# Kernel tuning notes

Measured on AMD Instinct MI355X. Metric: run time of the kernel, lower is better.

## Reference

```python
import jax, jax.numpy as jnp
import numpy as np

DMODEL = 512
NUM_HEADS = 8
HEAD_DIM = DMODEL // NUM_HEADS


def setup_inputs() -> dict:
    key = jax.random.key(0)
    k1, k2, k3, k4, k5 = jax.random.split(key, 5)
    x = jax.random.normal(k1, (4, 2048, DMODEL), dtype=jnp.float32)
    s = 1.0 / np.sqrt(DMODEL)
    W_qkv = jax.random.uniform(k2, (DMODEL, 3 * DMODEL), jnp.float32, -s, s)
    b_qkv = jax.random.uniform(k3, (3 * DMODEL,), jnp.float32, -s, s)
    W_out = jax.random.uniform(k4, (DMODEL, DMODEL), jnp.float32, -s, s)
    b_out = jax.random.uniform(k5, (DMODEL,), jnp.float32, -s, s)
    return {"x": x, "W_qkv": W_qkv, "b_qkv": b_qkv, "W_out": W_out, "b_out": b_out}


def reference(x, W_qkv, b_qkv, W_out, b_out):
    B, T, D = x.shape
    H, Hd = NUM_HEADS, HEAD_DIM
    qkv = x @ W_qkv + b_qkv                      # [B, T, 3D]
    qkv = qkv.reshape(B, T, 3, H, Hd).transpose(2, 0, 3, 1, 4)  # [3, B, H, T, Hd]
    q, k, v = qkv[0], qkv[1], qkv[2]
    scores = jnp.einsum('bhqd,bhkd->bhqk', q, k) / np.sqrt(Hd)  # [B, H, T, T]
    causal = jnp.tril(jnp.ones((T, T), dtype=bool))
    scores = jnp.where(causal, scores, -jnp.inf)
    weights = jax.nn.softmax(scores, axis=-1)
    out = jnp.einsum('bhqk,bhkd->bhqd', weights, v)  # [B, H, T, Hd]
    out = out.transpose(0, 2, 1, 3).reshape(B, T, D)
    return out @ W_out + b_out
```

## Files before the change

### kernel.cpp

```cpp
#include <hip/hip_runtime.h>
#include <cstdint>
#include <cstddef>

#define D_MODEL 512
#define SEQ_T 2048
#define NHEADS 8
#define HDIM 64

typedef __attribute__((ext_vector_type(8))) short bf16x8;
typedef __attribute__((ext_vector_type(4))) float f32x4;

__device__ __forceinline__ unsigned short f2bf(float f) {
  unsigned int u = __float_as_uint(f);
  u += 0x7FFFu + ((u >> 16) & 1u);
  return (unsigned short)(u >> 16);
}

__device__ __forceinline__ unsigned int pack_bf16(float lo, float hi) {
  unsigned int a = __float_as_uint(lo) + 0x8000u;
  unsigned int b = __float_as_uint(hi) + 0x8000u;
  return __builtin_amdgcn_perm(b, a, 0x07060302u);
}

#define QSCALE 0.18033688011112043f
#define SSHIFT 16.0f

__device__ __forceinline__ void async_lds16(const unsigned short* g,
                                            unsigned short* l) {
  __builtin_amdgcn_global_load_lds(
      (const __attribute__((address_space(1))) void*)g,
      (__attribute__((address_space(3))) void*)l, 16, 0, 0);
}

__global__ __launch_bounds__(256) void prep_kernel(
    const float* __restrict__ x, const float* __restrict__ W_qkv,
    const float* __restrict__ W_out, unsigned short* __restrict__ xb,
    unsigned short* __restrict__ Wqkt, unsigned short* __restrict__ Wot) {
  __shared__ float tile[64][65];
  const int bid = blockIdx.x;
  if (bid < 2048) {
    int i = (bid * 256 + threadIdx.x) * 8;
    float4 a = *(const float4*)(x + i);
    float4 b = *(const float4*)(x + i + 4);
    ushort4 lo = {f2bf(a.x), f2bf(a.y), f2bf(a.z), f2bf(a.w)};
    ushort4 hi = {f2bf(b.x), f2bf(b.y), f2bf(b.z), f2bf(b.w)};
    *(ushort4*)(xb + i) = lo;
    *(ushort4*)(xb + i + 4) = hi;
    return;
  }
  const float* src;
  unsigned short* dst;
  int R = 512, C, c0, r0;
  if (bid < 2048 + 192) {
    int t = bid - 2048;
    C = 1536; c0 = (t % 24) * 64; r0 = (t / 24) * 64;
    src = W_qkv; dst = Wqkt;
  } else {
    int t = bid - 2240;
    C = 512; c0 = (t & 7) * 64; r0 = (t >> 3) * 64;
    src = W_out; dst = Wot;
  }
  for (int i = threadIdx.x; i < 64 * 64; i += 256) {
    int r = i >> 6, c = i & 63;
    tile[r][c] = src[(size_t)(r0 + r) * C + c0 + c];
  }
  __syncthreads();
  for (int i = threadIdx.x; i < 64 * 64; i += 256) {
    int c = i >> 6, r = i & 63;
    dst[(size_t)(c0 + c) * R + r0 + r] = f2bf(tile[r][c]);
  }
}

__global__ __launch_bounds__(256) void gemm_qkv_mfma(
    const unsigned short* __restrict__ xb, const unsigned short* __restrict__ Wt,
    const float* __restrict__ bias, unsigned short* __restrict__ Qtb,
    unsigned short* __restrict__ Kb, unsigned short* __restrict__ Vtb) {
  __shared__ unsigned short As[128 * 64];
  __shared__ unsigned short Bs[128 * 64];
  const int tid = threadIdx.x;
  const int w = tid >> 6, lane = tid & 63;
  const int quad = lane >> 4, l15 = lane & 15;
  const int wm = w >> 1, wn = w & 1;
  const int m0 = blockIdx.x * 128, n0 = blockIdx.y * 128;

  const int srow = tid >> 3;
  const int schunk = (tid & 7) ^ (srow & 7);
  const unsigned short* ga = xb + (size_t)(m0 + srow) * 512 + schunk * 8;
  const unsigned short* gb = Wt + (size_t)(n0 + srow) * 512 + schunk * 8;
  unsigned short* lA = As + tid * 8;
  unsigned short* lB = Bs + tid * 8;

  f32x4 acc[4][4] = {};
  for (int k0 = 0; k0 < 512; k0 += 64) {
#pragma unroll
    for (int rr = 0; rr < 4; ++rr) {
      async_lds16(ga + (size_t)rr * 32 * 512 + k0, lA + rr * 2048);
      async_lds16(gb + (size_t)rr * 32 * 512 + k0, lB + rr * 2048);
    }
    __syncthreads();
    bf16x8 af[4][2], bfr[4][2];
#pragma unroll
    for (int mb = 0; mb < 4; ++mb) {
      int row = wm * 64 + mb * 16 + l15;
#pragma unroll
      for (int kk = 0; kk < 2; ++kk) {
        int slot = (kk * 4 + quad) ^ (row & 7);
        af[mb][kk] = *(const bf16x8*)&As[row * 64 + slot * 8];
      }
    }
#pragma unroll
    for (int nb = 0; nb < 4; ++nb) {
      int row = wn * 64 + nb * 16 + l15;
#pragma unroll
      for (int kk = 0; kk < 2; ++kk) {
        int slot = (kk * 4 + quad) ^ (row & 7);
        bfr[nb][kk] = *(const bf16x8*)&Bs[row * 64 + slot * 8];
      }
    }
#pragma unroll
    for (int mb = 0; mb < 4; ++mb)
#pragma unroll
      for (int nb = 0; nb < 4; ++nb) {
        acc[mb][nb] = __builtin_amdgcn_mfma_f32_16x16x32_bf16(
            af[mb][0], bfr[nb][0], acc[mb][nb], 0, 0, 0);
        acc[mb][nb] = __builtin_amdgcn_mfma_f32_16x16x32_bf16(
            af[mb][1], bfr[nb][1], acc[mb][nb], 0, 0, 0);
      }
    __syncthreads();
  }

  const int cbase = n0 + wn * 64;
  const int three = cbase >> 9;
  const int h = (cbase >> 6) & 7;
  const int bh = ((m0 >> 11) << 3) + h;
  const int t0 = (m0 & 2047) + wm * 64;
  float bv[4];
#pragma unroll
  for (int nb = 0; nb < 4; ++nb) bv[nb] = bias[cbase + nb * 16 + l15];

  if (three == 0) {
#pragma unroll
    for (int mb = 0; mb < 4; ++mb)
#pragma unroll
      for (int nb = 0; nb < 4; ++nb) {
        int trow = t0 + mb * 16 + quad * 4;
        ushort4 v = {f2bf((acc[mb][nb][0] + bv[nb]) * QSCALE),
                     f2bf((acc[mb][nb][1] + bv[nb]) * QSCALE),
                     f2bf((acc[mb][nb][2] + bv[nb]) * QSCALE),
                     f2bf((acc[mb][nb][3] + bv[nb]) * QSCALE)};
        *(ushort4*)(Qtb + ((size_t)bh * HDIM + nb * 16 + l15) * SEQ_T + trow) = v;
      }
  } else if (three == 2) {
#pragma unroll
    for (int mb = 0; mb < 4; ++mb)
#pragma unroll
      for (int nb = 0; nb < 4; ++nb) {
        int trow = t0 + mb * 16 + quad * 4;
        ushort4 v = {f2bf(acc[mb][nb][0] + bv[nb]), f2bf(acc[mb][nb][1] + bv[nb]),
                     f2bf(acc[mb][nb][2] + bv[nb]), f2bf(acc[mb][nb][3] + bv[nb])};
        *(ushort4*)(Vtb + ((size_t)bh * HDIM + nb * 16 + l15) * SEQ_T + trow) = v;
      }
  } else {
#pragma unroll
    for (int mb = 0; mb < 4; ++mb)
#pragma unroll
      for (int nb = 0; nb < 4; ++nb)
#pragma unroll
        for (int r = 0; r < 4; ++r) {
          int trow = t0 + mb * 16 + quad * 4 + r;
          Kb[((size_t)bh * SEQ_T + trow) * HDIM + nb * 16 + l15] =
              f2bf(acc[mb][nb][r] + bv[nb]);
        }
  }
}

__global__ __launch_bounds__(256, 4) void attn_mfma5(
    const unsigned short* __restrict__ Qtb, const unsigned short* __restrict__ Kb,
    const unsigned short* __restrict__ Vtb, unsigned short* __restrict__ AOb) {
  __shared__ __align__(16) unsigned short Ks[2][64 * 64];
  __shared__ __align__(16) unsigned short Vs[2][64 * 64];
  __shared__ __align__(16) unsigned short Pt[4][16 * 64];
  const int tid = threadIdx.x;
  const int w = tid >> 6, lane = tid & 63;
  const int quad = lane >> 4, l15 = lane & 15;

  const int bid = blockIdx.x;
  const int xcd = bid & 7;
  const int j = bid >> 3;
  const int c = j & 31, g = j >> 5;
  const int k = c >> 2;
  const int bh = xcd + 8 * (c & 3);
  const int qt = (g == 0) ? (31 - k) : (g == 1) ? (16 + k)
               : (g == 2) ? (15 - k) : k;

  const unsigned short* kbase = Kb + (size_t)bh * SEQ_T * HDIM;
  const unsigned short* vbase = Vtb + (size_t)bh * HDIM * SEQ_T;
  const int sr = tid >> 3;
  const int lc = tid & 7;
  const int scol = lc * 8;
  const int swc = (lc ^ (sr & 7)) * 8;

  bf16x8 qf0, qf1;
  {
    unsigned short qraw[16];
    const unsigned short* qp =
        Qtb + ((size_t)bh * HDIM + quad * 8) * SEQ_T + qt * 64 + w * 16 + l15;
#pragma unroll
    for (int jj = 0; jj < 8; ++jj) {
      qraw[jj] = qp[(size_t)jj * SEQ_T];
      qraw[8 + jj] = qp[(size_t)(32 + jj) * SEQ_T];
    }
    qf0 = *(const bf16x8*)qraw;
    qf1 = *(const bf16x8*)(qraw + 8);
  }
  const short oneb = (short)0x3F80;
  const bf16x8 ones = {oneb, oneb, oneb, oneb, oneb, oneb, oneb, oneb};

  f32x4 O[4] = {{0.f, 0.f, 0.f, 0.f}, {0.f, 0.f, 0.f, 0.f},
                {0.f, 0.f, 0.f, 0.f}, {0.f, 0.f, 0.f, 0.f}};
  f32x4 l_acc = {0.f, 0.f, 0.f, 0.f};
  const int q_rel = w * 16 + l15;
  const int r7 = l15 & 7;

  uint4 rk0, rk1, rv0, rv1;
  {
    const unsigned short* kp = kbase + (size_t)sr * 64 + scol;
    rk0 = *(const uint4*)kp;
    rk1 = *(const uint4*)(kp + 32 * 64);
    const unsigned short* vp = vbase + (size_t)sr * SEQ_T + scol;
    rv0 = *(const uint4*)vp;
    rv1 = *(const uint4*)(vp + 32 * SEQ_T);
  }
  *(uint4*)&Ks[0][sr * 64 + swc] = rk0;
  *(uint4*)&Ks[0][(sr + 32) * 64 + swc] = rk1;
  *(uint4*)&Vs[0][sr * 64 + swc] = rv0;
  *(uint4*)&Vs[0][(sr + 32) * 64 + swc] = rv1;
  __syncthreads();

  for (int i = 0; i < qt; ++i) {
    const int cur = i & 1;
    {
      const int nkt = i + 1;
      const unsigned short* kp = kbase + (size_t)(nkt * 64 + sr) * 64 + scol;
      rk0 = *(const uint4*)kp;
      rk1 = *(const uint4*)(kp + 32 * 64);
      const unsigned short* vp = vbase + (size_t)sr * SEQ_T + nkt * 64 + scol;
      rv0 = *(const uint4*)vp;
      rv1 = *(const uint4*)(vp + 32 * SEQ_T);
    }

    f32x4 S[4];
#pragma unroll
    for (int nb = 0; nb < 4; ++nb) {
      const int row = nb * 16 + l15;
      const unsigned short* k0p = &Ks[cur][row * 64 + ((quad ^ r7) * 8)];
      const unsigned short* k1p = &Ks[cur][row * 64 + (((quad + 4) ^ r7) * 8)];
      f32x4 z = {0.f, 0.f, 0.f, 0.f};
      z = __builtin_amdgcn_mfma_f32_16x16x32_bf16(*(const bf16x8*)k0p, qf0, z,
                                                  0, 0, 0);
      S[nb] = __builtin_amdgcn_mfma_f32_16x16x32_bf16(*(const bf16x8*)k1p, qf1,
                                                      z, 0, 0, 0);
    }

#pragma unroll
    for (int nb = 0; nb < 4; ++nb) {
      float p0 = __builtin_amdgcn_exp2f(S[nb][0] - SSHIFT);
      float p1 = __builtin_amdgcn_exp2f(S[nb][1] - SSHIFT);
      float p2 = __builtin_amdgcn_exp2f(S[nb][2] - SSHIFT);
      float p3 = __builtin_amdgcn_exp2f(S[nb][3] - SSHIFT);
      int cc = 2 * nb + (quad >> 1);
      uint2 pk = {pack_bf16(p0, p1), pack_bf16(p2, p3)};
      *(uint2*)&Pt[w][l15 * 64 + ((cc ^ r7) * 8) + (quad & 1) * 4] = pk;
    }

    bf16x8 pb0 = *(const bf16x8*)&Pt[w][l15 * 64 + ((quad ^ r7) * 8)];
    bf16x8 pb1 = *(const bf16x8*)&Pt[w][l15 * 64 + (((quad + 4) ^ r7) * 8)];
    l_acc = __builtin_amdgcn_mfma_f32_16x16x32_bf16(ones, pb0, l_acc, 0, 0, 0);
    l_acc = __builtin_amdgcn_mfma_f32_16x16x32_bf16(ones, pb1, l_acc, 0, 0, 0);
#pragma unroll
    for (int nbd = 0; nbd < 4; ++nbd) {
      const int row = nbd * 16 + l15;
      const unsigned short* v0p = &Vs[cur][row * 64 + ((quad ^ r7) * 8)];
      const unsigned short* v1p = &Vs[cur][row * 64 + (((quad + 4) ^ r7) * 8)];
      O[nbd] = __builtin_amdgcn_mfma_f32_16x16x32_bf16(*(const bf16x8*)v0p, pb0,
                                                       O[nbd], 0, 0, 0);
      O[nbd] = __builtin_amdgcn_mfma_f32_16x16x32_bf16(*(const bf16x8*)v1p, pb1,
                                                       O[nbd], 0, 0, 0);
    }

    const int nxt = cur ^ 1;
    *(uint4*)&Ks[nxt][sr * 64 + swc] = rk0;
    *(uint4*)&Ks[nxt][(sr + 32) * 64 + swc] = rk1;
    *(uint4*)&Vs[nxt][sr * 64 + swc] = rv0;
    *(uint4*)&Vs[nxt][(sr + 32) * 64 + swc] = rv1;
    __syncthreads();
  }

  {
    const int cur = qt & 1;
    const int nb_lim = w + 1;
    f32x4 S[4];
#pragma unroll
    for (int nb = 0; nb < 4; ++nb) {
      if (nb < nb_lim) {
        const int row = nb * 16 + l15;
        const unsigned short* k0p = &Ks[cur][row * 64 + ((quad ^ r7) * 8)];
        const unsigned short* k1p =
            &Ks[cur][row * 64 + (((quad + 4) ^ r7) * 8)];
        f32x4 z = {0.f, 0.f, 0.f, 0.f};
        z = __builtin_amdgcn_mfma_f32_16x16x32_bf16(*(const bf16x8*)k0p, qf0,
                                                    z, 0, 0, 0);
        S[nb] = __builtin_amdgcn_mfma_f32_16x16x32_bf16(*(const bf16x8*)k1p,
                                                        qf1, z, 0, 0, 0);
      }
    }
#pragma unroll
    for (int nb = 0; nb < 4; ++nb) {
      int cc = 2 * nb + (quad >> 1);
      if (nb < nb_lim) {
        float pp[4];
#pragma unroll
        for (int r = 0; r < 4; ++r) {
          float p = __builtin_amdgcn_exp2f(S[nb][r] - SSHIFT);
          int key_rel = nb * 16 + quad * 4 + r;
          pp[r] = (key_rel > q_rel) ? 0.f : p;
        }
        uint2 pk = {pack_bf16(pp[0], pp[1]), pack_bf16(pp[2], pp[3])};
        *(uint2*)&Pt[w][l15 * 64 + ((cc ^ r7) * 8) + (quad & 1) * 4] = pk;
      } else {
        uint2 z2 = {0u, 0u};
        *(uint2*)&Pt[w][l15 * 64 + ((cc ^ r7) * 8) + (quad & 1) * 4] = z2;
      }
    }
    const int kpv = (w >= 2) ? 2 : 1;
    bf16x8 pb0 = *(const bf16x8*)&Pt[w][l15 * 64 + ((quad ^ r7) * 8)];
    bf16x8 pb1 = *(const bf16x8*)&Pt[w][l15 * 64 + (((quad + 4) ^ r7) * 8)];
    l_acc = __builtin_amdgcn_mfma_f32_16x16x32_bf16(ones, pb0, l_acc, 0, 0, 0);
    if (kpv == 2)
      l_acc =
          __builtin_amdgcn_mfma_f32_16x16x32_bf16(ones, pb1, l_acc, 0, 0, 0);
#pragma unroll
    for (int nbd = 0; nbd < 4; ++nbd) {
      const int row = nbd * 16 + l15;
      const unsigned short* v0p = &Vs[cur][row * 64 + ((quad ^ r7) * 8)];
      O[nbd] = __builtin_amdgcn_mfma_f32_16x16x32_bf16(*(const bf16x8*)v0p, pb0,
                                                       O[nbd], 0, 0, 0);
      if (kpv == 2) {
        const unsigned short* v1p =
            &Vs[cur][row * 64 + (((quad + 4) ^ r7) * 8)];
        O[nbd] = __builtin_amdgcn_mfma_f32_16x16x32_bf16(*(const bf16x8*)v1p,
                                                         pb1, O[nbd], 0, 0, 0);
      }
    }
  }

  float inv = 1.0f / l_acc[0];
  const int bb = bh >> 3, h = bh & 7;
  int qrow = qt * 64 + q_rel;
  unsigned short* dst = AOb + ((size_t)bb * SEQ_T + qrow) * D_MODEL + (h << 6);
#pragma unroll
  for (int nbd = 0; nbd < 4; ++nbd) {
    ushort4 o4 = {f2bf(O[nbd][0] * inv), f2bf(O[nbd][1] * inv),
                  f2bf(O[nbd][2] * inv), f2bf(O[nbd][3] * inv)};
    *(ushort4*)(dst + nbd * 16 + quad * 4) = o4;
  }
}

__global__ __launch_bounds__(256) void gemm_out_mfma(
    const unsigned short* __restrict__ AOb, const unsigned short* __restrict__ Wot,
    const float* __restrict__ bias, float* __restrict__ out) {
  __shared__ unsigned short As[64 * 64];
  __shared__ unsigned short Bs[128 * 64];
  const int tid = threadIdx.x;
  const int w = tid >> 6, lane = tid & 63;
  const int quad = lane >> 4, l15 = lane & 15;
  const int m0 = blockIdx.x * 64, n0 = blockIdx.y * 128;

  const int srow = tid >> 3;
  const int schunk = (tid & 7) ^ (srow & 7);
  const unsigned short* ga = AOb + (size_t)(m0 + srow) * 512 + schunk * 8;
  const unsigned short* gb = Wot + (size_t)(n0 + srow) * 512 + schunk * 8;
  unsigned short* lA = As + tid * 8;
  unsigned short* lB = Bs + tid * 8;

  f32x4 acc[4][2] = {};
  for (int k0 = 0; k0 < 512; k0 += 64) {
#pragma unroll
    for (int rr = 0; rr < 2; ++rr)
      async_lds16(ga + (size_t)rr * 32 * 512 + k0, lA + rr * 2048);
#pragma unroll
    for (int rr = 0; rr < 4; ++rr)
      async_lds16(gb + (size_t)rr * 32 * 512 + k0, lB + rr * 2048);
    __syncthreads();
    bf16x8 af[4][2], bfr[2][2];
#pragma unroll
    for (int mb = 0; mb < 4; ++mb) {
      int row = mb * 16 + l15;
#pragma unroll
      for (int kk = 0; kk < 2; ++kk) {
        int slot = (kk * 4 + quad) ^ (row & 7);
        af[mb][kk] = *(const bf16x8*)&As[row * 64 + slot * 8];
      }
    }
#pragma unroll
    for (int nb = 0; nb < 2; ++nb) {
      int row = w * 32 + nb * 16 + l15;
#pragma unroll
      for (int kk = 0; kk < 2; ++kk) {
        int slot = (kk * 4 + quad) ^ (row & 7);
        bfr[nb][kk] = *(const bf16x8*)&Bs[row * 64 + slot * 8];
      }
    }
#pragma unroll
    for (int mb = 0; mb < 4; ++mb)
#pragma unroll
      for (int nb = 0; nb < 2; ++nb) {
        acc[mb][nb] = __builtin_amdgcn_mfma_f32_16x16x32_bf16(
            af[mb][0], bfr[nb][0], acc[mb][nb], 0, 0, 0);
        acc[mb][nb] = __builtin_amdgcn_mfma_f32_16x16x32_bf16(
            af[mb][1], bfr[nb][1], acc[mb][nb], 0, 0, 0);
      }
    __syncthreads();
  }

  const int cbase = n0 + w * 32;
  float bv[2];
#pragma unroll
  for (int nb = 0; nb < 2; ++nb) bv[nb] = bias[cbase + nb * 16 + l15];
#pragma unroll
  for (int mb = 0; mb < 4; ++mb)
#pragma unroll
    for (int nb = 0; nb < 2; ++nb)
#pragma unroll
      for (int r = 0; r < 4; ++r)
        out[(size_t)(m0 + mb * 16 + quad * 4 + r) * 512 + cbase + nb * 16 +
            l15] = acc[mb][nb][r] + bv[nb];
}

extern "C" void kernel_launch(void* const* d_in, const int* in_sizes, int n_in,
                              void* d_out, int out_size, void* d_ws,
                              size_t ws_size, hipStream_t stream) {
  const float* x     = (const float*)d_in[0];
  const float* W_qkv = (const float*)d_in[1];
  const float* b_qkv = (const float*)d_in[2];
  const float* W_out = (const float*)d_in[3];
  const float* b_out = (const float*)d_in[4];
  float* out = (float*)d_out;

  const size_t NX = (size_t)4 * SEQ_T * D_MODEL;
  unsigned short* xb   = (unsigned short*)d_ws;
  unsigned short* Wqkt = xb + NX;
  unsigned short* Wot  = Wqkt + (size_t)1536 * 512;
  unsigned short* Qtb  = Wot + (size_t)512 * 512;
  unsigned short* Kb   = Qtb + NX;
  unsigned short* Vtb  = Kb + NX;
  unsigned short* AOb  = Vtb + NX;

  prep_kernel<<<2304, 256, 0, stream>>>(x, W_qkv, W_out, xb, Wqkt, Wot);
  gemm_qkv_mfma<<<dim3(64, 12), 256, 0, stream>>>(xb, Wqkt, b_qkv, Qtb, Kb,
                                                  Vtb);
  attn_mfma5<<<dim3(1024), 256, 0, stream>>>(Qtb, Kb, Vtb, AOb);
  gemm_out_mfma<<<dim3(128, 4), 256, 0, stream>>>(AOb, Wot, b_out, out);
}
```

Baseline: 132.8 us.

## Process two query tiles per attention block to reuse K/V tiles

Each attention block now handles 128 query rows (two 64-row sub-tiles) against each staged K/V tile, so every K/V tile loaded into LDS feeds twice the MFMA work and the grid is halved. The causal diagonal is handled with per-subtile modes: masked, skipped or full. The aim is to cut global K/V traffic and LDS staging per query. In exchange the kernel uses twice the accumulator and P-tile LDS, its occupancy hint drops to 3, and with half as many blocks the load balancing across CUs gets coarser.

Result: slower. 143.4 us (+8.0%).

```diff
diff --git a/kernel.cpp b/kernel.cpp
--- a/kernel.cpp
+++ b/kernel.cpp
@@ -174,24 +174,23 @@
   }
 }
 
-__global__ __launch_bounds__(256, 4) void attn_mfma5(
+__global__ __launch_bounds__(256, 3) void attn_mfma6(
     const unsigned short* __restrict__ Qtb, const unsigned short* __restrict__ Kb,
     const unsigned short* __restrict__ Vtb, unsigned short* __restrict__ AOb) {
   __shared__ __align__(16) unsigned short Ks[2][64 * 64];
   __shared__ __align__(16) unsigned short Vs[2][64 * 64];
-  __shared__ __align__(16) unsigned short Pt[4][16 * 64];
+  __shared__ __align__(16) unsigned short Pt[4 * 2048];
   const int tid = threadIdx.x;
   const int w = tid >> 6, lane = tid & 63;
   const int quad = lane >> 4, l15 = lane & 15;
 
   const int bid = blockIdx.x;
   const int xcd = bid & 7;
-  const int j = bid >> 3;
-  const int c = j & 31, g = j >> 5;
-  const int k = c >> 2;
+  const int rest = bid >> 3;
+  const int c = rest & 31, g = rest >> 5;
   const int bh = xcd + 8 * (c & 3);
-  const int qt = (g == 0) ? (31 - k) : (g == 1) ? (16 + k)
-               : (g == 2) ? (15 - k) : k;
+  const int kq = c >> 2;
+  const int qt = g ? kq : (15 - kq);
 
   const unsigned short* kbase = Kb + (size_t)bh * SEQ_T * HDIM;
   const unsigned short* vbase = Vtb + (size_t)bh * HDIM * SEQ_T;
@@ -200,27 +199,33 @@
   const int scol = lc * 8;
   const int swc = (lc ^ (sr & 7)) * 8;
 
-  bf16x8 qf0, qf1;
-  {
+  bf16x8 qf[2][2];
+#pragma unroll
+  for (int h = 0; h < 2; ++h) {
     unsigned short qraw[16];
-    const unsigned short* qp =
-        Qtb + ((size_t)bh * HDIM + quad * 8) * SEQ_T + qt * 64 + w * 16 + l15;
+    const unsigned short* qp = Qtb + ((size_t)bh * HDIM + quad * 8) * SEQ_T +
+                               qt * 128 + h * 64 + w * 16 + l15;
 #pragma unroll
     for (int jj = 0; jj < 8; ++jj) {
       qraw[jj] = qp[(size_t)jj * SEQ_T];
       qraw[8 + jj] = qp[(size_t)(32 + jj) * SEQ_T];
     }
-    qf0 = *(const bf16x8*)qraw;
-    qf1 = *(const bf16x8*)(qraw + 8);
+    qf[h][0] = *(const bf16x8*)qraw;
+    qf[h][1] = *(const bf16x8*)(qraw + 8);
   }
   const short oneb = (short)0x3F80;
   const bf16x8 ones = {oneb, oneb, oneb, oneb, oneb, oneb, oneb, oneb};
 
-  f32x4 O[4] = {{0.f, 0.f, 0.f, 0.f}, {0.f, 0.f, 0.f, 0.f},
-                {0.f, 0.f, 0.f, 0.f}, {0.f, 0.f, 0.f, 0.f}};
-  f32x4 l_acc = {0.f, 0.f, 0.f, 0.f};
+  f32x4 O[2][4];
+  f32x4 l_acc[2];
+#pragma unroll
+  for (int h = 0; h < 2; ++h) {
+    l_acc[h] = (f32x4){0.f, 0.f, 0.f, 0.f};
+#pragma unroll
+    for (int nbd = 0; nbd < 4; ++nbd) O[h][nbd] = (f32x4){0.f, 0.f, 0.f, 0.f};
+  }
   const int q_rel = w * 16 + l15;
-  const int r7 = l15 & 7;
+  const int r7m = l15 & 7;
 
   uint4 rk0, rk1, rv0, rv1;
   {
@@ -237,132 +242,142 @@
   *(uint4*)&Vs[0][(sr + 32) * 64 + swc] = rv1;
   __syncthreads();
 
-  for (int i = 0; i < qt; ++i) {
-    const int cur = i & 1;
-    {
-      const int nkt = i + 1;
-      const unsigned short* kp = kbase + (size_t)(nkt * 64 + sr) * 64 + scol;
-      rk0 = *(const uint4*)kp;
-      rk1 = *(const uint4*)(kp + 32 * 64);
-      const unsigned short* vp = vbase + (size_t)sr * SEQ_T + nkt * 64 + scol;
-      rv0 = *(const uint4*)vp;
-      rv1 = *(const uint4*)(vp + 32 * SEQ_T);
-    }
-
-    f32x4 S[4];
-#pragma unroll
-    for (int nb = 0; nb < 4; ++nb) {
-      const int row = nb * 16 + l15;
-      const unsigned short* k0p = &Ks[cur][row * 64 + ((quad ^ r7) * 8)];
-      const unsigned short* k1p = &Ks[cur][row * 64 + (((quad + 4) ^ r7) * 8)];
-      f32x4 z = {0.f, 0.f, 0.f, 0.f};
-      z = __builtin_amdgcn_mfma_f32_16x16x32_bf16(*(const bf16x8*)k0p, qf0, z,
-                                                  0, 0, 0);
-      S[nb] = __builtin_amdgcn_mfma_f32_16x16x32_bf16(*(const bf16x8*)k1p, qf1,
-                                                      z, 0, 0, 0);
-    }
-
-#pragma unroll
-    for (int nb = 0; nb < 4; ++nb) {
-      float p0 = __builtin_amdgcn_exp2f(S[nb][0] - SSHIFT);
-      float p1 = __builtin_amdgcn_exp2f(S[nb][1] - SSHIFT);
-      float p2 = __builtin_amdgcn_exp2f(S[nb][2] - SSHIFT);
-      float p3 = __builtin_amdgcn_exp2f(S[nb][3] - SSHIFT);
-      int cc = 2 * nb + (quad >> 1);
-      uint2 pk = {pack_bf16(p0, p1), pack_bf16(p2, p3)};
-      *(uint2*)&Pt[w][l15 * 64 + ((cc ^ r7) * 8) + (quad & 1) * 4] = pk;
-    }
-
-    bf16x8 pb0 = *(const bf16x8*)&Pt[w][l15 * 64 + ((quad ^ r7) * 8)];
-    bf16x8 pb1 = *(const bf16x8*)&Pt[w][l15 * 64 + (((quad + 4) ^ r7) * 8)];
-    l_acc = __builtin_amdgcn_mfma_f32_16x16x32_bf16(ones, pb0, l_acc, 0, 0, 0);
-    l_acc = __builtin_amdgcn_mfma_f32_16x16x32_bf16(ones, pb1, l_acc, 0, 0, 0);
-#pragma unroll
-    for (int nbd = 0; nbd < 4; ++nbd) {
-      const int row = nbd * 16 + l15;
-      const unsigned short* v0p = &Vs[cur][row * 64 + ((quad ^ r7) * 8)];
-      const unsigned short* v1p = &Vs[cur][row * 64 + (((quad + 4) ^ r7) * 8)];
-      O[nbd] = __builtin_amdgcn_mfma_f32_16x16x32_bf16(*(const bf16x8*)v0p, pb0,
-                                                       O[nbd], 0, 0, 0);
-      O[nbd] = __builtin_amdgcn_mfma_f32_16x16x32_bf16(*(const bf16x8*)v1p, pb1,
-                                                       O[nbd], 0, 0, 0);
-    }
-
-    const int nxt = cur ^ 1;
+  auto prefetch = [&](int nkt) {
+    const unsigned short* kp = kbase + (size_t)(nkt * 64 + sr) * 64 + scol;
+    rk0 = *(const uint4*)kp;
+    rk1 = *(const uint4*)(kp + 32 * 64);
+    const unsigned short* vp = vbase + (size_t)sr * SEQ_T + nkt * 64 + scol;
+    rv0 = *(const uint4*)vp;
+    rv1 = *(const uint4*)(vp + 32 * SEQ_T);
+  };
+  auto commit = [&](int nxt) {
     *(uint4*)&Ks[nxt][sr * 64 + swc] = rk0;
     *(uint4*)&Ks[nxt][(sr + 32) * 64 + swc] = rk1;
     *(uint4*)&Vs[nxt][sr * 64 + swc] = rv0;
     *(uint4*)&Vs[nxt][(sr + 32) * 64 + swc] = rv1;
-    __syncthreads();
-  }
-
-  {
-    const int cur = qt & 1;
-    const int nb_lim = w + 1;
-    f32x4 S[4];
+  };
+
+  auto tile_body = [&](int cur, int mode0, int mode1) {
+    const int lim0 = (mode0 == 2) ? 0 : ((mode0 == 1) ? (w + 1) : 4);
+    const int lim1 = (mode1 == 2) ? 0 : ((mode1 == 1) ? (w + 1) : 4);
+    f32x4 S0[4], S1[4];
 #pragma unroll
     for (int nb = 0; nb < 4; ++nb) {
-      if (nb < nb_lim) {
-        const int row = nb * 16 + l15;
-        const unsigned short* k0p = &Ks[cur][row * 64 + ((quad ^ r7) * 8)];
-        const unsigned short* k1p =
-            &Ks[cur][row * 64 + (((quad + 4) ^ r7) * 8)];
+      const int row = nb * 16 + l15;
+      bf16x8 k0 = *(const bf16x8*)&Ks[cur][row * 64 + ((quad ^ r7m) * 8)];
+      bf16x8 k1 = *(const bf16x8*)&Ks[cur][row * 64 + (((quad + 4) ^ r7m) * 8)];
+      if (nb < lim0) {
         f32x4 z = {0.f, 0.f, 0.f, 0.f};
-        z = __builtin_amdgcn_mfma_f32_16x16x32_bf16(*(const bf16x8*)k0p, qf0,
-                                                    z, 0, 0, 0);
-        S[nb] = __builtin_amdgcn_mfma_f32_16x16x32_bf16(*(const bf16x8*)k1p,
-                                                        qf1, z, 0, 0, 0);
-      }
-    }
-#pragma unroll
-    for (int nb = 0; nb < 4; ++nb) {
-      int cc = 2 * nb + (quad >> 1);
-      if (nb < nb_lim) {
-        float pp[4];
-#pragma unroll
-        for (int r = 0; r < 4; ++r) {
-          float p = __builtin_amdgcn_exp2f(S[nb][r] - SSHIFT);
-          int key_rel = nb * 16 + quad * 4 + r;
-          pp[r] = (key_rel > q_rel) ? 0.f : p;
+        z = __builtin_amdgcn_mfma_f32_16x16x32_bf16(k0, qf[0][0], z, 0, 0, 0);
+        S0[nb] = __builtin_amdgcn_mfma_f32_16x16x32_bf16(k1, qf[0][1], z, 0, 0, 0);
+      }
+      if (nb < lim1) {
+        f32x4 z = {0.f, 0.f, 0.f, 0.f};
+        z = __builtin_amdgcn_mfma_f32_16x16x32_bf16(k0, qf[1][0], z, 0, 0, 0);
+        S1[nb] = __builtin_amdgcn_mfma_f32_16x16x32_bf16(k1, qf[1][1], z, 0, 0, 0);
+      }
+    }
+#pragma unroll
+    for (int h = 0; h < 2; ++h) {
+      f32x4* S = h ? S1 : S0;
+      const int lim = h ? lim1 : lim0;
+      const int mode = h ? mode1 : mode0;
+#pragma unroll
+      for (int nb = 0; nb < 4; ++nb) {
+        int cc = 2 * nb + (quad >> 1);
+        unsigned short* base = &Pt[w * 2048 + h * 1024 + l15 * 64 +
+                                   ((cc ^ r7m) * 8) + (quad & 1) * 4];
+        if (nb < lim) {
+          float pp[4];
+#pragma unroll
+          for (int r = 0; r < 4; ++r) {
+            float p = __builtin_amdgcn_exp2f(S[nb][r] - SSHIFT);
+            if (mode == 1) {
+              int key_rel = nb * 16 + quad * 4 + r;
+              if (key_rel > q_rel) p = 0.f;
+            }
+            pp[r] = p;
+          }
+          uint2 pk = {pack_bf16(pp[0], pp[1]), pack_bf16(pp[2], pp[3])};
+          *(uint2*)base = pk;
+        } else if (mode == 1) {
+          uint2 z2 = {0u, 0u};
+          *(uint2*)base = z2;
         }
-        uint2 pk = {pack_bf16(pp[0], pp[1]), pack_bf16(pp[2], pp[3])};
-        *(uint2*)&Pt[w][l15 * 64 + ((cc ^ r7) * 8) + (quad & 1) * 4] = pk;
-      } else {
-        uint2 z2 = {0u, 0u};
-        *(uint2*)&Pt[w][l15 * 64 + ((cc ^ r7) * 8) + (quad & 1) * 4] = z2;
-      }
-    }
-    const int kpv = (w >= 2) ? 2 : 1;
-    bf16x8 pb0 = *(const bf16x8*)&Pt[w][l15 * 64 + ((quad ^ r7) * 8)];
-    bf16x8 pb1 = *(const bf16x8*)&Pt[w][l15 * 64 + (((quad + 4) ^ r7) * 8)];
-    l_acc = __builtin_amdgcn_mfma_f32_16x16x32_bf16(ones, pb0, l_acc, 0, 0, 0);
-    if (kpv == 2)
-      l_acc =
-          __builtin_amdgcn_mfma_f32_16x16x32_bf16(ones, pb1, l_acc, 0, 0, 0);
+      }
+    }
+    bf16x8 pb[2][2];
+    const int kpv0 = (mode0 == 1 && w < 2) ? 1 : 2;
+    const int kpv1 = (mode1 == 1 && w < 2) ? 1 : 2;
+    if (mode0 != 2) {
+      pb[0][0] = *(const bf16x8*)&Pt[w * 2048 + l15 * 64 + ((quad ^ r7m) * 8)];
+      pb[0][1] =
+          *(const bf16x8*)&Pt[w * 2048 + l15 * 64 + (((quad + 4) ^ r7m) * 8)];
+      l_acc[0] =
+          __builtin_amdgcn_mfma_f32_16x16x32_bf16(ones, pb[0][0], l_acc[0], 0, 0, 0);
+      if (kpv0 == 2)
+        l_acc[0] = __builtin_amdgcn_mfma_f32_16x16x32_bf16(ones, pb[0][1],
+                                                           l_acc[0], 0, 0, 0);
+    }
+    if (mode1 != 2) {
+      pb[1][0] =
+          *(const bf16x8*)&Pt[w * 2048 + 1024 + l15 * 64 + ((quad ^ r7m) * 8)];
+      pb[1][1] = *(const bf16x8*)&Pt[w * 2048 + 1024 + l15 * 64 +
+                                     (((quad + 4) ^ r7m) * 8)];
+      l_acc[1] =
+          __builtin_amdgcn_mfma_f32_16x16x32_bf16(ones, pb[1][0], l_acc[1], 0, 0, 0);
+      if (kpv1 == 2)
+        l_acc[1] = __builtin_amdgcn_mfma_f32_16x16x32_bf16(ones, pb[1][1],
+                                                           l_acc[1], 0, 0, 0);
+    }
 #pragma unroll
     for (int nbd = 0; nbd < 4; ++nbd) {
       const int row = nbd * 16 + l15;
-      const unsigned short* v0p = &Vs[cur][row * 64 + ((quad ^ r7) * 8)];
-      O[nbd] = __builtin_amdgcn_mfma_f32_16x16x32_bf16(*(const bf16x8*)v0p, pb0,
-                                                       O[nbd], 0, 0, 0);
-      if (kpv == 2) {
-        const unsigned short* v1p =
-            &Vs[cur][row * 64 + (((quad + 4) ^ r7) * 8)];
-        O[nbd] = __builtin_amdgcn_mfma_f32_16x16x32_bf16(*(const bf16x8*)v1p,
-                                                         pb1, O[nbd], 0, 0, 0);
-      }
-    }
-  }
-
-  float inv = 1.0f / l_acc[0];
-  const int bb = bh >> 3, h = bh & 7;
-  int qrow = qt * 64 + q_rel;
-  unsigned short* dst = AOb + ((size_t)bb * SEQ_T + qrow) * D_MODEL + (h << 6);
-#pragma unroll
-  for (int nbd = 0; nbd < 4; ++nbd) {
-    ushort4 o4 = {f2bf(O[nbd][0] * inv), f2bf(O[nbd][1] * inv),
-                  f2bf(O[nbd][2] * inv), f2bf(O[nbd][3] * inv)};
-    *(ushort4*)(dst + nbd * 16 + quad * 4) = o4;
+      bf16x8 v0 = *(const bf16x8*)&Vs[cur][row * 64 + ((quad ^ r7m) * 8)];
+      bf16x8 v1 = *(const bf16x8*)&Vs[cur][row * 64 + (((quad + 4) ^ r7m) * 8)];
+      if (mode0 != 2) {
+        O[0][nbd] = __builtin_amdgcn_mfma_f32_16x16x32_bf16(v0, pb[0][0],
+                                                            O[0][nbd], 0, 0, 0);
+        if (kpv0 == 2)
+          O[0][nbd] = __builtin_amdgcn_mfma_f32_16x16x32_bf16(
+              v1, pb[0][1], O[0][nbd], 0, 0, 0);
+      }
+      if (mode1 != 2) {
+        O[1][nbd] = __builtin_amdgcn_mfma_f32_16x16x32_bf16(v0, pb[1][0],
+                                                            O[1][nbd], 0, 0, 0);
+        if (kpv1 == 2)
+          O[1][nbd] = __builtin_amdgcn_mfma_f32_16x16x32_bf16(
+              v1, pb[1][1], O[1][nbd], 0, 0, 0);
+      }
+    }
+  };
+
+  for (int i = 0; i < 2 * qt; ++i) {
+    const int cur = i & 1;
+    prefetch(i + 1);
+    tile_body(cur, 0, 0);
+    commit(cur ^ 1);
+    __syncthreads();
+  }
+  prefetch(2 * qt + 1);
+  tile_body(0, 1, 0);
+  commit(1);
+  __syncthreads();
+  tile_body(1, 2, 1);
+
+  const int bb = bh >> 3, h8 = bh & 7;
+#pragma unroll
+  for (int h = 0; h < 2; ++h) {
+    float inv = 1.0f / l_acc[h][0];
+    int qrow = qt * 128 + h * 64 + q_rel;
+    unsigned short* dst =
+        AOb + ((size_t)bb * SEQ_T + qrow) * D_MODEL + (h8 << 6);
+#pragma unroll
+    for (int nbd = 0; nbd < 4; ++nbd) {
+      ushort4 o4 = {f2bf(O[h][nbd][0] * inv), f2bf(O[h][nbd][1] * inv),
+                    f2bf(O[h][nbd][2] * inv), f2bf(O[h][nbd][3] * inv)};
+      *(ushort4*)(dst + nbd * 16 + quad * 4) = o4;
+    }
   }
 }
 
@@ -459,6 +474,6 @@
   prep_kernel<<<2304, 256, 0, stream>>>(x, W_qkv, W_out, xb, Wqkt, Wot);
   gemm_qkv_mfma<<<dim3(64, 12), 256, 0, stream>>>(xb, Wqkt, b_qkv, Qtb, Kb,
                                                   Vtb);
-  attn_mfma5<<<dim3(1024), 256, 0, stream>>>(Qtb, Kb, Vtb, AOb);
+  attn_mfma6<<<dim3(512), 256, 0, stream>>>(Qtb, Kb, Vtb, AOb);
   gemm_out_mfma<<<dim3(128, 4), 256, 0, stream>>>(AOb, Wot, b_out, out);
 }
```

## Split attention key tiles across waves and keep P in registers

Applied to the files above, without the earlier changes.

The attention kernel now gives each wave one 16-key slice of every 64-key tile for all 64 queries, where before each wave owned 16 queries over all keys. The softmax probabilities feed a 16x16x16 MFMA straight from registers, which removes the per-wave LDS round-trip for P and the ones-matrix MFMA used for row sums. The diagonal tile is folded into the main loop with masking. The cost is a cross-wave reduction of O and l through shared memory at the end, more registers (launch bounds lowered from 4 to 3 blocks), and more MFMA instructions for the PV product.

Result: slower. 142.3 us (+7.1%).

```diff
diff --git a/kernel.cpp b/kernel.cpp
--- a/kernel.cpp
+++ b/kernel.cpp
@@ -8,6 +8,7 @@
 #define HDIM 64
 
 typedef __attribute__((ext_vector_type(8))) short bf16x8;
+typedef __attribute__((ext_vector_type(4))) short bf16x4;
 typedef __attribute__((ext_vector_type(4))) float f32x4;
 
 __device__ __forceinline__ unsigned short f2bf(float f) {
@@ -174,12 +175,11 @@
   }
 }
 
-__global__ __launch_bounds__(256, 4) void attn_mfma5(
+__global__ __launch_bounds__(256, 3) void attn_mfma7(
     const unsigned short* __restrict__ Qtb, const unsigned short* __restrict__ Kb,
     const unsigned short* __restrict__ Vtb, unsigned short* __restrict__ AOb) {
-  __shared__ __align__(16) unsigned short Ks[2][64 * 64];
-  __shared__ __align__(16) unsigned short Vs[2][64 * 64];
-  __shared__ __align__(16) unsigned short Pt[4][16 * 64];
+  __shared__ __align__(16) unsigned short KVs[4][64 * 64];
+  __shared__ float ls[4 * 64];
   const int tid = threadIdx.x;
   const int w = tid >> 6, lane = tid & 63;
   const int quad = lane >> 4, l15 = lane & 15;
@@ -200,27 +200,33 @@
   const int scol = lc * 8;
   const int swc = (lc ^ (sr & 7)) * 8;
 
-  bf16x8 qf0, qf1;
-  {
-    unsigned short qraw[16];
-    const unsigned short* qp =
-        Qtb + ((size_t)bh * HDIM + quad * 8) * SEQ_T + qt * 64 + w * 16 + l15;
-#pragma unroll
-    for (int jj = 0; jj < 8; ++jj) {
-      qraw[jj] = qp[(size_t)jj * SEQ_T];
-      qraw[8 + jj] = qp[(size_t)(32 + jj) * SEQ_T];
-    }
-    qf0 = *(const bf16x8*)qraw;
-    qf1 = *(const bf16x8*)(qraw + 8);
-  }
-  const short oneb = (short)0x3F80;
-  const bf16x8 ones = {oneb, oneb, oneb, oneb, oneb, oneb, oneb, oneb};
-
-  f32x4 O[4] = {{0.f, 0.f, 0.f, 0.f}, {0.f, 0.f, 0.f, 0.f},
-                {0.f, 0.f, 0.f, 0.f}, {0.f, 0.f, 0.f, 0.f}};
-  f32x4 l_acc = {0.f, 0.f, 0.f, 0.f};
-  const int q_rel = w * 16 + l15;
-  const int r7 = l15 & 7;
+  bf16x8 qf[4][2];
+#pragma unroll
+  for (int qb = 0; qb < 4; ++qb) {
+#pragma unroll
+    for (int h = 0; h < 2; ++h) {
+      unsigned short qraw[8];
+      const unsigned short* qp = Qtb +
+          ((size_t)bh * HDIM + h * 32 + quad * 8) * SEQ_T + qt * 64 + qb * 16 +
+          l15;
+#pragma unroll
+      for (int jj = 0; jj < 8; ++jj) qraw[jj] = qp[(size_t)jj * SEQ_T];
+      qf[qb][h] = *(const bf16x8*)qraw;
+    }
+  }
+
+  f32x4 O[4][4];
+#pragma unroll
+  for (int dvb = 0; dvb < 4; ++dvb)
+#pragma unroll
+    for (int qb = 0; qb < 4; ++qb) O[dvb][qb] = (f32x4){0.f, 0.f, 0.f, 0.f};
+  float l4[4] = {0.f, 0.f, 0.f, 0.f};
+
+  const int myrowK = w * 16 + l15;
+  const int kc0 = (quad ^ (myrowK & 7)) * 8;
+  const int kc1 = ((quad + 4) ^ (myrowK & 7)) * 8;
+  const int vchunk = 2 * w + (quad >> 1);
+  const int vsub = (quad & 1) * 4;
 
   uint4 rk0, rk1, rv0, rv1;
   {
@@ -231,15 +237,17 @@
     rv0 = *(const uint4*)vp;
     rv1 = *(const uint4*)(vp + 32 * SEQ_T);
   }
-  *(uint4*)&Ks[0][sr * 64 + swc] = rk0;
-  *(uint4*)&Ks[0][(sr + 32) * 64 + swc] = rk1;
-  *(uint4*)&Vs[0][sr * 64 + swc] = rv0;
-  *(uint4*)&Vs[0][(sr + 32) * 64 + swc] = rv1;
+  *(uint4*)&KVs[0][sr * 64 + swc] = rk0;
+  *(uint4*)&KVs[0][(sr + 32) * 64 + swc] = rk1;
+  *(uint4*)&KVs[2][sr * 64 + swc] = rv0;
+  *(uint4*)&KVs[2][(sr + 32) * 64 + swc] = rv1;
   __syncthreads();
 
-  for (int i = 0; i < qt; ++i) {
+  for (int i = 0; i <= qt; ++i) {
     const int cur = i & 1;
-    {
+    const bool diag = (i == qt);
+
+    if (i < qt) {
       const int nkt = i + 1;
       const unsigned short* kp = kbase + (size_t)(nkt * 64 + sr) * 64 + scol;
       rk0 = *(const uint4*)kp;
@@ -249,120 +257,99 @@
       rv1 = *(const uint4*)(vp + 32 * SEQ_T);
     }
 
-    f32x4 S[4];
-#pragma unroll
-    for (int nb = 0; nb < 4; ++nb) {
-      const int row = nb * 16 + l15;
-      const unsigned short* k0p = &Ks[cur][row * 64 + ((quad ^ r7) * 8)];
-      const unsigned short* k1p = &Ks[cur][row * 64 + (((quad + 4) ^ r7) * 8)];
-      f32x4 z = {0.f, 0.f, 0.f, 0.f};
-      z = __builtin_amdgcn_mfma_f32_16x16x32_bf16(*(const bf16x8*)k0p, qf0, z,
-                                                  0, 0, 0);
-      S[nb] = __builtin_amdgcn_mfma_f32_16x16x32_bf16(*(const bf16x8*)k1p, qf1,
-                                                      z, 0, 0, 0);
-    }
-
-#pragma unroll
-    for (int nb = 0; nb < 4; ++nb) {
-      float p0 = __builtin_amdgcn_exp2f(S[nb][0] - SSHIFT);
-      float p1 = __builtin_amdgcn_exp2f(S[nb][1] - SSHIFT);
-      float p2 = __builtin_amdgcn_exp2f(S[nb][2] - SSHIFT);
-      float p3 = __builtin_amdgcn_exp2f(S[nb][3] - SSHIFT);
-      int cc = 2 * nb + (quad >> 1);
-      uint2 pk = {pack_bf16(p0, p1), pack_bf16(p2, p3)};
-      *(uint2*)&Pt[w][l15 * 64 + ((cc ^ r7) * 8) + (quad & 1) * 4] = pk;
-    }
-
-    bf16x8 pb0 = *(const bf16x8*)&Pt[w][l15 * 64 + ((quad ^ r7) * 8)];
-    bf16x8 pb1 = *(const bf16x8*)&Pt[w][l15 * 64 + (((quad + 4) ^ r7) * 8)];
-    l_acc = __builtin_amdgcn_mfma_f32_16x16x32_bf16(ones, pb0, l_acc, 0, 0, 0);
-    l_acc = __builtin_amdgcn_mfma_f32_16x16x32_bf16(ones, pb1, l_acc, 0, 0, 0);
-#pragma unroll
-    for (int nbd = 0; nbd < 4; ++nbd) {
-      const int row = nbd * 16 + l15;
-      const unsigned short* v0p = &Vs[cur][row * 64 + ((quad ^ r7) * 8)];
-      const unsigned short* v1p = &Vs[cur][row * 64 + (((quad + 4) ^ r7) * 8)];
-      O[nbd] = __builtin_amdgcn_mfma_f32_16x16x32_bf16(*(const bf16x8*)v0p, pb0,
-                                                       O[nbd], 0, 0, 0);
-      O[nbd] = __builtin_amdgcn_mfma_f32_16x16x32_bf16(*(const bf16x8*)v1p, pb1,
-                                                       O[nbd], 0, 0, 0);
-    }
-
-    const int nxt = cur ^ 1;
-    *(uint4*)&Ks[nxt][sr * 64 + swc] = rk0;
-    *(uint4*)&Ks[nxt][(sr + 32) * 64 + swc] = rk1;
-    *(uint4*)&Vs[nxt][sr * 64 + swc] = rv0;
-    *(uint4*)&Vs[nxt][(sr + 32) * 64 + swc] = rv1;
+    bf16x8 kf0 = *(const bf16x8*)&KVs[cur][myrowK * 64 + kc0];
+    bf16x8 kf1 = *(const bf16x8*)&KVs[cur][myrowK * 64 + kc1];
+    bf16x4 vf[4];
+#pragma unroll
+    for (int dvb = 0; dvb < 4; ++dvb) {
+      int row = dvb * 16 + l15;
+      vf[dvb] = *(const bf16x4*)&KVs[2 + cur][row * 64 +
+                                             ((vchunk ^ (row & 7)) * 8) + vsub];
+    }
+
+#pragma unroll
+    for (int qb = 0; qb < 4; ++qb) {
+      f32x4 S = {0.f, 0.f, 0.f, 0.f};
+      S = __builtin_amdgcn_mfma_f32_16x16x32_bf16(kf0, qf[qb][0], S, 0, 0, 0);
+      S = __builtin_amdgcn_mfma_f32_16x16x32_bf16(kf1, qf[qb][1], S, 0, 0, 0);
+      float pp[4];
+#pragma unroll
+      for (int r = 0; r < 4; ++r) {
+        float p = __builtin_amdgcn_exp2f(S[r] - SSHIFT);
+        if (diag) {
+          int key_rel = w * 16 + quad * 4 + r;
+          int q_rel = qb * 16 + l15;
+          if (key_rel > q_rel) p = 0.f;
+        }
+        pp[r] = p;
+      }
+      l4[qb] += pp[0] + pp[1] + pp[2] + pp[3];
+      uint2 pk = {pack_bf16(pp[0], pp[1]), pack_bf16(pp[2], pp[3])};
+      bf16x4 pf = *(const bf16x4*)&pk;
+#pragma unroll
+      for (int dvb = 0; dvb < 4; ++dvb)
+        O[dvb][qb] = __builtin_amdgcn_mfma_f32_16x16x16bf16_1k(
+            vf[dvb], pf, O[dvb][qb], 0, 0, 0);
+    }
+
+    if (i < qt) {
+      const int nxt = cur ^ 1;
+      *(uint4*)&KVs[nxt][sr * 64 + swc] = rk0;
+      *(uint4*)&KVs[nxt][(sr + 32) * 64 + swc] = rk1;
+      *(uint4*)&KVs[2 + nxt][sr * 64 + swc] = rv0;
+      *(uint4*)&KVs[2 + nxt][(sr + 32) * 64 + swc] = rv1;
+    }
     __syncthreads();
   }
 
-  {
-    const int cur = qt & 1;
-    const int nb_lim = w + 1;
-    f32x4 S[4];
-#pragma unroll
-    for (int nb = 0; nb < 4; ++nb) {
-      if (nb < nb_lim) {
-        const int row = nb * 16 + l15;
-        const unsigned short* k0p = &Ks[cur][row * 64 + ((quad ^ r7) * 8)];
-        const unsigned short* k1p =
-            &Ks[cur][row * 64 + (((quad + 4) ^ r7) * 8)];
-        f32x4 z = {0.f, 0.f, 0.f, 0.f};
-        z = __builtin_amdgcn_mfma_f32_16x16x32_bf16(*(const bf16x8*)k0p, qf0,
-                                                    z, 0, 0, 0);
-        S[nb] = __builtin_amdgcn_mfma_f32_16x16x32_bf16(*(const bf16x8*)k1p,
-                                                        qf1, z, 0, 0, 0);
-      }
-    }
-#pragma unroll
-    for (int nb = 0; nb < 4; ++nb) {
-      int cc = 2 * nb + (quad >> 1);
-      if (nb < nb_lim) {
-        float pp[4];
-#pragma unroll
-        for (int r = 0; r < 4; ++r) {
-          float p = __builtin_amdgcn_exp2f(S[nb][r] - SSHIFT);
-          int key_rel = nb * 16 + quad * 4 + r;
-          pp[r] = (key_rel > q_rel) ? 0.f : p;
-        }
-        uint2 pk = {pack_bf16(pp[0], pp[1]), pack_bf16(pp[2], pp[3])};
-        *(uint2*)&Pt[w][l15 * 64 + ((cc ^ r7) * 8) + (quad & 1) * 4] = pk;
-      } else {
-        uint2 z2 = {0u, 0u};
-        *(uint2*)&Pt[w][l15 * 64 + ((cc ^ r7) * 8) + (quad & 1) * 4] = z2;
-      }
-    }
-    const int kpv = (w >= 2) ? 2 : 1;
-    bf16x8 pb0 = *(const bf16x8*)&Pt[w][l15 * 64 + ((quad ^ r7) * 8)];
-    bf16x8 pb1 = *(const bf16x8*)&Pt[w][l15 * 64 + (((quad + 4) ^ r7) * 8)];
-    l_acc = __builtin_amdgcn_mfma_f32_16x16x32_bf16(ones, pb0, l_acc, 0, 0, 0);
-    if (kpv == 2)
-      l_acc =
-          __builtin_amdgcn_mfma_f32_16x16x32_bf16(ones, pb1, l_acc, 0, 0, 0);
-#pragma unroll
-    for (int nbd = 0; nbd < 4; ++nbd) {
-      const int row = nbd * 16 + l15;
-      const unsigned short* v0p = &Vs[cur][row * 64 + ((quad ^ r7) * 8)];
-      O[nbd] = __builtin_amdgcn_mfma_f32_16x16x32_bf16(*(const bf16x8*)v0p, pb0,
-                                                       O[nbd], 0, 0, 0);
-      if (kpv == 2) {
-        const unsigned short* v1p =
-            &Vs[cur][row * 64 + (((quad + 4) ^ r7) * 8)];
-        O[nbd] = __builtin_amdgcn_mfma_f32_16x16x32_bf16(*(const bf16x8*)v1p,
-                                                         pb1, O[nbd], 0, 0, 0);
-      }
-    }
-  }
-
-  float inv = 1.0f / l_acc[0];
-  const int bb = bh >> 3, h = bh & 7;
-  int qrow = qt * 64 + q_rel;
-  unsigned short* dst = AOb + ((size_t)bb * SEQ_T + qrow) * D_MODEL + (h << 6);
-#pragma unroll
-  for (int nbd = 0; nbd < 4; ++nbd) {
-    ushort4 o4 = {f2bf(O[nbd][0] * inv), f2bf(O[nbd][1] * inv),
-                  f2bf(O[nbd][2] * inv), f2bf(O[nbd][3] * inv)};
-    *(ushort4*)(dst + nbd * 16 + quad * 4) = o4;
+#pragma unroll
+  for (int qb = 0; qb < 4; ++qb) {
+    float v = l4[qb];
+    v += __shfl_xor(v, 16);
+    v += __shfl_xor(v, 32);
+    l4[qb] = v;
+  }
+  if (quad == 0) {
+#pragma unroll
+    for (int qb = 0; qb < 4; ++qb) ls[w * 64 + qb * 16 + l15] = l4[qb];
+  }
+  float* Ored = (float*)&KVs[0][0];
+  auto oslot = [&](int slot, int dvb, int qb) {
+    return Ored + ((((slot * 4 + dvb) * 4 + qb) * 64) + lane) * 4;
+  };
+  if (w < 2) {
+#pragma unroll
+    for (int dvb = 0; dvb < 4; ++dvb)
+#pragma unroll
+      for (int qb = 0; qb < 4; ++qb) *(f32x4*)oslot(w, dvb, qb) = O[dvb][qb];
+  }
+  __syncthreads();
+  if (w >= 2) {
+    const int slot = w - 2;
+#pragma unroll
+    for (int dvb = 0; dvb < 4; ++dvb)
+#pragma unroll
+      for (int qb = 0; qb < 4; ++qb) {
+        f32x4 t = *(const f32x4*)oslot(slot, dvb, qb);
+        t += O[dvb][qb];
+        *(f32x4*)oslot(slot, dvb, qb) = t;
+      }
+  }
+  __syncthreads();
+
+  const int bb = bh >> 3, h8 = bh & 7;
+#pragma unroll
+  for (int qb = 0; qb < 4; ++qb) {
+    f32x4 a = *(const f32x4*)oslot(0, w, qb);
+    f32x4 b = *(const f32x4*)oslot(1, w, qb);
+    float lt = ls[0 * 64 + qb * 16 + l15] + ls[1 * 64 + qb * 16 + l15] +
+               ls[2 * 64 + qb * 16 + l15] + ls[3 * 64 + qb * 16 + l15];
+    float inv = 1.0f / lt;
+    int qrow = qt * 64 + qb * 16 + l15;
+    ushort4 o4 = {f2bf((a[0] + b[0]) * inv), f2bf((a[1] + b[1]) * inv),
+                  f2bf((a[2] + b[2]) * inv), f2bf((a[3] + b[3]) * inv)};
+    *(ushort4*)(AOb + ((size_t)bb * SEQ_T + qrow) * D_MODEL + (h8 << 6) +
+                w * 16 + quad * 4) = o4;
   }
 }
 
@@ -459,6 +446,6 @@
   prep_kernel<<<2304, 256, 0, stream>>>(x, W_qkv, W_out, xb, Wqkt, Wot);
   gemm_qkv_mfma<<<dim3(64, 12), 256, 0, stream>>>(xb, Wqkt, b_qkv, Qtb, Kb,
                                                   Vtb);
-  attn_mfma5<<<dim3(1024), 256, 0, stream>>>(Qtb, Kb, Vtb, AOb);
+  attn_mfma7<<<dim3(1024), 256, 0, stream>>>(Qtb, Kb, Vtb, AOb);
   gemm_out_mfma<<<dim3(128, 4), 256, 0, stream>>>(AOb, Wot, b_out, out);
 }
```
